# Optimization experiments

Measured on AMD Instinct MI355X. Metric: run time of the kernel, lower is better.

Reference implementation:

```python
import jax, jax.numpy as jnp
import numpy as np

NUM_HEADS = 32
NUM_KV_HEADS = 8
HEAD_DIM = 128
GROUPS = NUM_HEADS // NUM_KV_HEADS  # 4
ROPE_BASE = 1000000.0


def _rope_cos_sin(seq_len, dtype):
    inv_freq = 1.0 / (ROPE_BASE ** (jnp.arange(0, HEAD_DIM, 2, dtype=jnp.float32) / HEAD_DIM))
    t = jnp.arange(seq_len, dtype=jnp.float32)
    freqs = jnp.einsum('i,j->ij', t, inv_freq)          # [S, D/2]
    emb = jnp.concatenate([freqs, freqs], axis=-1)       # [S, D]
    return jnp.cos(emb).astype(dtype), jnp.sin(emb).astype(dtype)


def _rotate_half(x):
    x1, x2 = jnp.split(x, 2, axis=-1)
    return jnp.concatenate([-x2, x1], axis=-1)


def setup_inputs() -> dict:
    key = jax.random.key(0)
    k1, k2, k3 = jax.random.split(key, 3)
    B, S, H = 1, 2048, 4096
    hidden_states = jax.random.normal(k1, (B, S, H), dtype=jnp.float32)
    wqkv = jax.random.normal(k2, (6144, H), dtype=jnp.float32) * (H ** -0.5)
    wo = jax.random.normal(k3, (H, H), dtype=jnp.float32) * (H ** -0.5)
    # causal additive mask [B, 1, S, S]
    neg = jnp.finfo(jnp.float32).min
    causal = jnp.triu(jnp.full((S, S), neg, dtype=jnp.float32), k=1)
    attention_mask = causal[None, None]
    position_ids = jnp.broadcast_to(jnp.arange(S, dtype=jnp.int64 if jax.config.jax_enable_x64 else jnp.int32), (B, S))
    return {'hidden_states': hidden_states, 'wqkv': wqkv, 'wo': wo,
            'attention_mask': attention_mask, 'position_ids': position_ids}


def reference(hidden_states, wqkv, wo, attention_mask, position_ids):
    B, S, _ = hidden_states.shape
    qkv = hidden_states @ wqkv.T                               # [B, S, 6144]
    qkv = qkv.reshape(B, S, NUM_KV_HEADS, GROUPS + 2, HEAD_DIM)
    q = qkv[..., :GROUPS, :].reshape(B, S, NUM_HEADS, HEAD_DIM)
    k = qkv[..., -2, :]                                        # [B, S, KVH, D]
    v = qkv[..., -1, :]
    q = q.transpose(0, 2, 1, 3)                                # [B, H, S, D]
    k = k.transpose(0, 2, 1, 3)                                # [B, KVH, S, D]
    v = v.transpose(0, 2, 1, 3)

    cos, sin = _rope_cos_sin(S, hidden_states.dtype)
    cos = cos[position_ids][:, None]                           # [B, 1, S, D]
    sin = sin[position_ids][:, None]
    q = q * cos + _rotate_half(q) * sin
    k = k * cos + _rotate_half(k) * sin

    # repeat_kv: [B, KVH, S, D] -> [B, H, S, D]
    k = jnp.repeat(k, GROUPS, axis=1)
    v = jnp.repeat(v, GROUPS, axis=1)

    scale = 1.0 / jnp.sqrt(jnp.asarray(HEAD_DIM, dtype=q.dtype))
    scores = jnp.einsum('bhqd,bhkd->bhqk', q, k) * scale + attention_mask
    probs = jax.nn.softmax(scores.astype(jnp.float32), axis=-1).astype(q.dtype)
    attn = jnp.einsum('bhqk,bhkd->bhqd', probs, v)             # [B, H, S, D]
    attn = attn.transpose(0, 2, 1, 3).reshape(B, S, NUM_HEADS * HEAD_DIM)
    return attn @ wo.T
```

## Files before the change

### kernel.cpp

```cpp
#include <hip/hip_runtime.h>
#include <stdint.h>

typedef unsigned short u16;
typedef unsigned int u32;
typedef short s16x8 __attribute__((ext_vector_type(8)));
typedef __bf16 bfv8 __attribute__((ext_vector_type(8)));
typedef float f32x4 __attribute__((ext_vector_type(4)));

#define S_LEN 2048
#define HID 4096
#define NQKV 6144

#define MFMA16(d, a, b) (d) = __builtin_amdgcn_mfma_f32_16x16x32_bf16((a), (b), (d), 0, 0, 0)

__device__ __forceinline__ u16 f2bf(float f){
  u32 u = __float_as_uint(f);
  return (u16)((u + 0x7fffu + ((u >> 16) & 1u)) >> 16);
}
__device__ __forceinline__ float bf2f(u16 x){
  return __uint_as_float((u32)x << 16);
}

__device__ __forceinline__ void gl16(const u16* g, u16* l){
  __builtin_amdgcn_global_load_lds((const __attribute__((address_space(1))) u32*)g,
                                   (__attribute__((address_space(3))) u32*)l,
                                   16, 0, 0);
}

__global__ __launch_bounds__(256) void cvt_bf16(const float* __restrict__ in,
                                                u16* __restrict__ out, int n4){
  int i = blockIdx.x * 256 + threadIdx.x;
  if (i >= n4) return;
  float4 v = ((const float4*)in)[i];
  ushort4 o;
  o.x = f2bf(v.x); o.y = f2bf(v.y); o.z = f2bf(v.z); o.w = f2bf(v.w);
  ((ushort4*)out)[i] = o;
}

template<typename OT>
__global__ __launch_bounds__(256) void gemm_bt(const u16* __restrict__ A,
                                               const u16* __restrict__ B,
                                               OT* __restrict__ C, int N, int K){
  __shared__ __align__(16) u16 As[2][128*32];
  __shared__ __align__(16) u16 Bs[2][128*32];
  const int tid = threadIdx.x;
  const int lane = tid & 63, wave = tid >> 6;
  const int g = lane >> 4, l16 = lane & 15;
  const int wr = wave >> 1, wc = wave & 1;
  const u16* Ag = A + (size_t)blockIdx.y * 128 * K;
  const u16* Bg = B + (size_t)blockIdx.x * 128 * K;
  const int r0 = wave*32 + (lane >> 2);
  const int r1 = r0 + 16;
  const int su = lane & 3;
  const int l0 = wave*1024;
  const int l1 = wave*1024 + 512;
  f32x4 acc[4][4] = {};

#define ISSUE(b, k0)                                          \
  gl16(Ag + (size_t)r0*K + (k0) + su*8, &As[b][l0]);          \
  gl16(Ag + (size_t)r1*K + (k0) + su*8, &As[b][l1]);          \
  gl16(Bg + (size_t)r0*K + (k0) + su*8, &Bs[b][l0]);          \
  gl16(Bg + (size_t)r1*K + (k0) + su*8, &Bs[b][l1]);

  ISSUE(0, 0)
  __syncthreads();
  const int KIT = K >> 5;
  for (int it = 0; it < KIT; it++){
    const int b = it & 1;
    if (it + 1 < KIT){ ISSUE(b^1, (it+1)*32) }
    bfv8 af[4], bfr[4];
    #pragma unroll
    for (int i = 0; i < 4; i++)
      af[i] = *(const bfv8*)&As[b][(wr*64 + i*16 + l16)*32 + g*8];
    #pragma unroll
    for (int j = 0; j < 4; j++)
      bfr[j] = *(const bfv8*)&Bs[b][(wc*64 + j*16 + l16)*32 + g*8];
    #pragma unroll
    for (int i = 0; i < 4; i++)
      #pragma unroll
      for (int j = 0; j < 4; j++)
        MFMA16(acc[i][j], af[i], bfr[j]);
    __syncthreads();
  }
#undef ISSUE
  OT* Cp = C + (size_t)(blockIdx.y*128 + wr*64) * N + blockIdx.x*128 + wc*64;
  #pragma unroll
  for (int i = 0; i < 4; i++)
    #pragma unroll
    for (int j = 0; j < 4; j++)
      #pragma unroll
      for (int r = 0; r < 4; r++){
        float v = acc[i][j][r];
        if constexpr (sizeof(OT) == 2)
          Cp[(size_t)(i*16 + g*4 + r) * N + j*16 + l16] = f2bf(v);
        else
          Cp[(size_t)(i*16 + g*4 + r) * N + j*16 + l16] = v;
      }
}

__global__ __launch_bounds__(256) void rope_reorg(const u16* __restrict__ qkv,
                                                  const int* __restrict__ pos,
                                                  u16* __restrict__ Qb, u16* __restrict__ Kb){
  const int hh = blockIdx.x;
  const int s  = blockIdx.y*4 + (threadIdx.x >> 6);
  const int j  = threadIdx.x & 63;
  const float p = (float)pos[s];
  const float inv = __expf(-(float)j * (13.815510557964274f / 64.0f));
  float sn, cs;
  sincosf(p * inv, &sn, &cs);
  const u16* src;
  u16* dst;
  if (hh < 32){
    src = qkv + (size_t)s*NQKV + (hh >> 2)*768 + (hh & 3)*128;
    dst = Qb + ((size_t)hh*S_LEN + s)*128;
  } else {
    int h = hh - 32;
    src = qkv + (size_t)s*NQKV + h*768 + 512;
    dst = Kb + ((size_t)h*S_LEN + s)*128;
  }
  float x1 = bf2f(src[j]), x2 = bf2f(src[j + 64]);
  dst[j]      = f2bf(x1*cs - x2*sn);
  dst[j + 64] = f2bf(x2*cs + x1*sn);
}

__global__ __launch_bounds__(256) void v_transpose(const u16* __restrict__ qkv,
                                                   u16* __restrict__ Vt){
  __shared__ u16 T[64][72];
  const int st = blockIdx.x, dt = blockIdx.y, h = blockIdx.z;
  const int w = threadIdx.x >> 6, lane = threadIdx.x & 63;
  const int s0 = st*64, d0 = dt*64;
  #pragma unroll
  for (int i = 0; i < 16; i++){
    int sl = w*16 + i;
    T[sl][lane] = qkv[(size_t)(s0+sl)*NQKV + h*768 + 640 + d0 + lane];
  }
  __syncthreads();
  #pragma unroll
  for (int i = 0; i < 16; i++){
    int dl = w*16 + i;
    Vt[((size_t)h*128 + d0 + dl)*S_LEN + s0 + lane] = T[lane][dl];
  }
}

__global__ __launch_bounds__(256) void attn_fwd(const u16* __restrict__ Q,
                                                const u16* __restrict__ K,
                                                const u16* __restrict__ V,
                                                u16* __restrict__ O){
  __shared__ __align__(16) u16 Ks[64*128];
  __shared__ __align__(16) u16 Vs[128*64];
  __shared__ __align__(16) u16 Ps[4][16][72];
  const int hq = blockIdx.x;
  const int qblk = 31 - blockIdx.y;
  const int hk = hq >> 2;
  const int tid = threadIdx.x, lane = tid & 63, w = tid >> 6;
  const int g = lane >> 4, l16 = lane & 15;
  const int q0 = qblk*64 + w*16;
  const u16* Qg = Q + ((size_t)hq*S_LEN + q0 + l16)*128;
  bfv8 qf[4];
  #pragma unroll
  for (int kk = 0; kk < 4; kk++) qf[kk] = *(const bfv8*)(Qg + kk*32 + g*8);
  const u16* Kg = K + (size_t)hk*S_LEN*128;
  const u16* Vg = V + (size_t)hk*128*S_LEN;
  f32x4 oacc[8] = {};
  float m_run[4], l_run[4];
  #pragma unroll
  for (int r = 0; r < 4; r++){ m_run[r] = -1e30f; l_run[r] = 0.0f; }
  const float scale = 0.08838834764831845f;

  const int rowk = w*16 + (lane >> 4);
  const int rowv = w*32 + (lane >> 3);

#define KV_LOAD(t, kr, vr)                                                        \
  _Pragma("unroll")                                                               \
  for (int i = 0; i < 4; i++){                                                    \
    kr[i] = *(const s16x8*)(Kg + ((size_t)((t)*64 + rowk + i*4))*128 + (lane & 15)*8); \
    vr[i] = *(const s16x8*)(Vg + (size_t)(rowv + i*8)*S_LEN + (t)*64 + (lane & 7)*8);  \
  }
#define KV_STORE(kr, vr)                                                          \
  _Pragma("unroll")                                                               \
  for (int i = 0; i < 4; i++){                                                    \
    int rk = rowk + i*4, rv = rowv + i*8;                                         \
    *(s16x8*)&Ks[rk*128 + ((lane & 15) ^ (rk & 7))*8] = kr[i];                    \
    *(s16x8*)&Vs[rv*64  + ((lane & 7)  ^ (rv & 7))*8] = vr[i];                    \
  }

  {
    s16x8 kr[4], vr[4];
    KV_LOAD(0, kr, vr)
    KV_STORE(kr, vr)
  }
  __syncthreads();

  for (int t = 0; t <= qblk; t++){
    s16x8 nkr[4], nvr[4];
    if (t + 1 <= qblk){ KV_LOAD(t+1, nkr, nvr) }
    f32x4 sacc[4] = {};
    #pragma unroll
    for (int j = 0; j < 4; j++){
      int row = j*16 + l16;
      #pragma unroll
      for (int kk = 0; kk < 4; kk++){
        bfv8 kf = *(const bfv8*)&Ks[row*128 + ((kk*4 + g) ^ (row & 7))*8];
        MFMA16(sacc[j], qf[kk], kf);
      }
    }
    float sc[4][4];
    #pragma unroll
    for (int j = 0; j < 4; j++)
      #pragma unroll
      for (int r = 0; r < 4; r++)
        sc[j][r] = sacc[j][r] * scale;
    if (t == qblk){
      #pragma unroll
      for (int j = 0; j < 4; j++){
        int kvc = t*64 + j*16 + l16;
        #pragma unroll
        for (int r = 0; r < 4; r++)
          if (kvc > q0 + g*4 + r) sc[j][r] = -1e30f;
      }
    }
    float mx[4];
    #pragma unroll
    for (int r = 0; r < 4; r++)
      mx[r] = fmaxf(fmaxf(sc[0][r], sc[1][r]), fmaxf(sc[2][r], sc[3][r]));
    #pragma unroll
    for (int off = 1; off < 16; off <<= 1)
      #pragma unroll
      for (int r = 0; r < 4; r++)
        mx[r] = fmaxf(mx[r], __shfl_xor(mx[r], off));
    float sf[4], pr[4][4], rsum[4];
    #pragma unroll
    for (int r = 0; r < 4; r++){
      float mn = fmaxf(m_run[r], mx[r]);
      sf[r] = __expf(m_run[r] - mn);
      m_run[r] = mn;
    }
    #pragma unroll
    for (int j = 0; j < 4; j++)
      #pragma unroll
      for (int r = 0; r < 4; r++)
        pr[j][r] = __expf(sc[j][r] - m_run[r]);
    #pragma unroll
    for (int r = 0; r < 4; r++)
      rsum[r] = (pr[0][r] + pr[1][r]) + (pr[2][r] + pr[3][r]);
    #pragma unroll
    for (int off = 1; off < 16; off <<= 1)
      #pragma unroll
      for (int r = 0; r < 4; r++)
        rsum[r] += __shfl_xor(rsum[r], off);
    #pragma unroll
    for (int r = 0; r < 4; r++)
      l_run[r] = l_run[r]*sf[r] + rsum[r];
    #pragma unroll
    for (int n = 0; n < 8; n++)
      #pragma unroll
      for (int r = 0; r < 4; r++)
        oacc[n][r] *= sf[r];
    #pragma unroll
    for (int j = 0; j < 4; j++)
      #pragma unroll
      for (int r = 0; r < 4; r++)
        Ps[w][g*4 + r][j*16 + l16] = f2bf(pr[j][r]);
    bfv8 pf[2];
    #pragma unroll
    for (int kk = 0; kk < 2; kk++)
      pf[kk] = *(const bfv8*)&Ps[w][l16][kk*32 + g*8];
    #pragma unroll
    for (int n = 0; n < 8; n++){
      int drow = n*16 + l16;
      #pragma unroll
      for (int kk = 0; kk < 2; kk++){
        bfv8 vf = *(const bfv8*)&Vs[drow*64 + ((kk*4 + g) ^ (drow & 7))*8];
        MFMA16(oacc[n], pf[kk], vf);
      }
    }
    __syncthreads();
    if (t + 1 <= qblk){ KV_STORE(nkr, nvr) }
    __syncthreads();
  }
#undef KV_LOAD
#undef KV_STORE
  #pragma unroll
  for (int r = 0; r < 4; r++){
    float invl = 1.0f / l_run[r];
    #pragma unroll
    for (int n = 0; n < 8; n++)
      O[(size_t)(q0 + g*4 + r)*HID + hq*128 + n*16 + l16] = f2bf(oacc[n][r]*invl);
  }
}

extern "C" void kernel_launch(void* const* d_in, const int* in_sizes, int n_in,
                              void* d_out, int out_size, void* d_ws, size_t ws_size,
                              hipStream_t stream){
  const float* hidden = (const float*)d_in[0];
  const float* wqkv   = (const float*)d_in[1];
  const float* wo     = (const float*)d_in[2];
  const int*   pos    = (const int*)d_in[4];
  float* out = (float*)d_out;
  char* ws = (char*)d_ws;

  u16* hB    = (u16*)(ws);
  u16* wqkvB = (u16*)(ws + (16ull<<20));
  u16* woB   = (u16*)(ws + (16ull<<20));
  u16* qkvB  = (u16*)(ws + (64ull<<20));
  u16* attnB = (u16*)(ws + (64ull<<20));
  u16* Qb    = (u16*)(ws + (88ull<<20));
  u16* Kb    = (u16*)(ws + (104ull<<20));
  u16* Vtb   = (u16*)(ws + (108ull<<20));

  cvt_bf16<<<dim3(8192),  256, 0, stream>>>(hidden, hB, 2097152);
  cvt_bf16<<<dim3(24576), 256, 0, stream>>>(wqkv, wqkvB, 6291456);
  gemm_bt<u16><<<dim3(48,16), 256, 0, stream>>>(hB, wqkvB, qkvB, NQKV, HID);
  cvt_bf16<<<dim3(16384), 256, 0, stream>>>(wo, woB, 4194304);
  rope_reorg<<<dim3(40,512), 256, 0, stream>>>(qkvB, pos, Qb, Kb);
  v_transpose<<<dim3(32,2,8), 256, 0, stream>>>(qkvB, Vtb);
  attn_fwd<<<dim3(32,32), 256, 0, stream>>>(Qb, Kb, Vtb, attnB);
  gemm_bt<float><<<dim3(32,16), 256, 0, stream>>>(attnB, woB, out, HID, HID);
}
```

Before: 542.0 us.

## Use native bf16 casts, fuse rope across heads, lazily rescale softmax

Replaces the manual round-to-nearest bf16 conversion with the compiler's native __bf16 cast, which may map to hardware conversion instructions. The rope kernel now computes sin/cos once per position and loops over all 40 Q/K heads, removing 40x redundant transcendental work, and switches to fast __sincosf. The attention kernel skips the online-softmax rescale of the accumulators unless the running max grows by more than 8, which saves multiplies but allows unnormalized exponentials up to e^8 in bf16 probabilities. The fused rope grid is much smaller (512 blocks), which reduces parallelism for that kernel.

Result: faster. 530.6 us (-2.1%).

```diff
diff --git a/kernel.cpp b/kernel.cpp
--- a/kernel.cpp
+++ b/kernel.cpp
@@ -13,9 +13,9 @@
 
 #define MFMA16(d, a, b) (d) = __builtin_amdgcn_mfma_f32_16x16x32_bf16((a), (b), (d), 0, 0, 0)
 
-__device__ __forceinline__ u16 f2bf(float f){
-  u32 u = __float_as_uint(f);
-  return (u16)((u + 0x7fffu + ((u >> 16) & 1u)) >> 16);
+__device__ __forceinline__ u16 f2b(float f){
+  __bf16 h = (__bf16)f;
+  return __builtin_bit_cast(u16, h);
 }
 __device__ __forceinline__ float bf2f(u16 x){
   return __uint_as_float((u32)x << 16);
@@ -33,7 +33,7 @@
   if (i >= n4) return;
   float4 v = ((const float4*)in)[i];
   ushort4 o;
-  o.x = f2bf(v.x); o.y = f2bf(v.y); o.z = f2bf(v.z); o.w = f2bf(v.w);
+  o.x = f2b(v.x); o.y = f2b(v.y); o.z = f2b(v.z); o.w = f2b(v.w);
   ((ushort4*)out)[i] = o;
 }
 
@@ -92,7 +92,7 @@
       for (int r = 0; r < 4; r++){
         float v = acc[i][j][r];
         if constexpr (sizeof(OT) == 2)
-          Cp[(size_t)(i*16 + g*4 + r) * N + j*16 + l16] = f2bf(v);
+          Cp[(size_t)(i*16 + g*4 + r) * N + j*16 + l16] = f2b(v);
         else
           Cp[(size_t)(i*16 + g*4 + r) * N + j*16 + l16] = v;
       }
@@ -101,26 +101,29 @@
 __global__ __launch_bounds__(256) void rope_reorg(const u16* __restrict__ qkv,
                                                   const int* __restrict__ pos,
                                                   u16* __restrict__ Qb, u16* __restrict__ Kb){
-  const int hh = blockIdx.x;
-  const int s  = blockIdx.y*4 + (threadIdx.x >> 6);
-  const int j  = threadIdx.x & 63;
+  const int s = blockIdx.x*4 + (threadIdx.x >> 6);
+  const int j = threadIdx.x & 63;
   const float p = (float)pos[s];
   const float inv = __expf(-(float)j * (13.815510557964274f / 64.0f));
   float sn, cs;
-  sincosf(p * inv, &sn, &cs);
-  const u16* src;
-  u16* dst;
-  if (hh < 32){
-    src = qkv + (size_t)s*NQKV + (hh >> 2)*768 + (hh & 3)*128;
-    dst = Qb + ((size_t)hh*S_LEN + s)*128;
-  } else {
-    int h = hh - 32;
-    src = qkv + (size_t)s*NQKV + h*768 + 512;
-    dst = Kb + ((size_t)h*S_LEN + s)*128;
-  }
-  float x1 = bf2f(src[j]), x2 = bf2f(src[j + 64]);
-  dst[j]      = f2bf(x1*cs - x2*sn);
-  dst[j + 64] = f2bf(x2*cs + x1*sn);
+  __sincosf(p * inv, &sn, &cs);
+  const u16* base = qkv + (size_t)s*NQKV;
+  #pragma unroll 4
+  for (int hh = 0; hh < 32; hh++){
+    const u16* src = base + (hh >> 2)*768 + (hh & 3)*128;
+    u16* dst = Qb + ((size_t)hh*S_LEN + s)*128;
+    float x1 = bf2f(src[j]), x2 = bf2f(src[j + 64]);
+    dst[j]      = f2b(x1*cs - x2*sn);
+    dst[j + 64] = f2b(x2*cs + x1*sn);
+  }
+  #pragma unroll 4
+  for (int h = 0; h < 8; h++){
+    const u16* src = base + h*768 + 512;
+    u16* dst = Kb + ((size_t)h*S_LEN + s)*128;
+    float x1 = bf2f(src[j]), x2 = bf2f(src[j + 64]);
+    dst[j]      = f2b(x1*cs - x2*sn);
+    dst[j + 64] = f2b(x2*cs + x1*sn);
+  }
 }
 
 __global__ __launch_bounds__(256) void v_transpose(const u16* __restrict__ qkv,
@@ -228,13 +231,25 @@
       #pragma unroll
       for (int r = 0; r < 4; r++)
         mx[r] = fmaxf(mx[r], __shfl_xor(mx[r], off));
-    float sf[4], pr[4][4], rsum[4];
-    #pragma unroll
-    for (int r = 0; r < 4; r++){
-      float mn = fmaxf(m_run[r], mx[r]);
-      sf[r] = __expf(m_run[r] - mn);
-      m_run[r] = mn;
+    bool need = false;
+    #pragma unroll
+    for (int r = 0; r < 4; r++) need |= (mx[r] > m_run[r] + 8.0f);
+    if (__any(need)){
+      float sf[4];
+      #pragma unroll
+      for (int r = 0; r < 4; r++){
+        float mn = fmaxf(m_run[r], mx[r]);
+        sf[r] = __expf(m_run[r] - mn);
+        m_run[r] = mn;
+        l_run[r] *= sf[r];
+      }
+      #pragma unroll
+      for (int n = 0; n < 8; n++)
+        #pragma unroll
+        for (int r = 0; r < 4; r++)
+          oacc[n][r] *= sf[r];
     }
+    float pr[4][4], rsum[4];
     #pragma unroll
     for (int j = 0; j < 4; j++)
       #pragma unroll
@@ -250,17 +265,12 @@
         rsum[r] += __shfl_xor(rsum[r], off);
     #pragma unroll
     for (int r = 0; r < 4; r++)
-      l_run[r] = l_run[r]*sf[r] + rsum[r];
-    #pragma unroll
-    for (int n = 0; n < 8; n++)
-      #pragma unroll
-      for (int r = 0; r < 4; r++)
-        oacc[n][r] *= sf[r];
-    #pragma unroll
-    for (int j = 0; j < 4; j++)
-      #pragma unroll
-      for (int r = 0; r < 4; r++)
-        Ps[w][g*4 + r][j*16 + l16] = f2bf(pr[j][r]);
+      l_run[r] += rsum[r];
+    #pragma unroll
+    for (int j = 0; j < 4; j++)
+      #pragma unroll
+      for (int r = 0; r < 4; r++)
+        Ps[w][g*4 + r][j*16 + l16] = f2b(pr[j][r]);
     bfv8 pf[2];
     #pragma unroll
     for (int kk = 0; kk < 2; kk++)
@@ -285,7 +295,7 @@
     float invl = 1.0f / l_run[r];
     #pragma unroll
     for (int n = 0; n < 8; n++)
-      O[(size_t)(q0 + g*4 + r)*HID + hq*128 + n*16 + l16] = f2bf(oacc[n][r]*invl);
+      O[(size_t)(q0 + g*4 + r)*HID + hq*128 + n*16 + l16] = f2b(oacc[n][r]*invl);
   }
 }
 
@@ -312,7 +322,7 @@
   cvt_bf16<<<dim3(24576), 256, 0, stream>>>(wqkv, wqkvB, 6291456);
   gemm_bt<u16><<<dim3(48,16), 256, 0, stream>>>(hB, wqkvB, qkvB, NQKV, HID);
   cvt_bf16<<<dim3(16384), 256, 0, stream>>>(wo, woB, 4194304);
-  rope_reorg<<<dim3(40,512), 256, 0, stream>>>(qkvB, pos, Qb, Kb);
+  rope_reorg<<<dim3(512), 256, 0, stream>>>(qkvB, pos, Qb, Kb);
   v_transpose<<<dim3(32,2,8), 256, 0, stream>>>(qkvB, Vtb);
   attn_fwd<<<dim3(32,32), 256, 0, stream>>>(Qb, Kb, Vtb, attnB);
   gemm_bt<float><<<dim3(32,16), 256, 0, stream>>>(attnB, woB, out, HID, HID);
```
